# Performance work log

Hardware: AMD Instinct MI355X
Metric: run time of the kernel (lower is better)

Reference implementation:

```python
import jax, jax.numpy as jnp
import numpy as np


def setup_inputs() -> dict:
    key = jax.random.key(0)
    k1, k2, k3, k4 = jax.random.split(key, 4)
    B, T, d_model, d_internal = 4, 2048, 1024, 64
    x = jax.random.normal(k1, (B, T, d_model), dtype=jnp.float32)
    # torch.nn.Linear weights: [out_features, in_features]
    s = 1.0 / np.sqrt(d_model)
    W_Q = jax.random.uniform(k2, (d_internal, d_model), jnp.float32, -s, s)
    W_K = jax.random.uniform(k3, (d_internal, d_model), jnp.float32, -s, s)
    W_V = jax.random.uniform(k4, (d_internal, d_model), jnp.float32, -s, s)
    return {"x": x, "W_Q": W_Q, "W_K": W_K, "W_V": W_V}


def reference(x, W_Q, W_K, W_V):
    B, T, C = x.shape  # C == d_model
    Q = jnp.einsum('btc,dc->btd', x, W_Q)
    K = jnp.einsum('btc,dc->btd', x, W_K)
    # Faithful to source bug: V is computed with W_K, W_V is unused.
    V = jnp.einsum('btc,dc->btd', x, W_K)
    scale = C ** (-0.5)  # source scales by d_model, not d_internal
    attn = jnp.einsum('btd,bsd->bts', Q, K) * scale  # [B,T,T]
    causal = jnp.tril(jnp.ones((T, T), dtype=bool))
    attn = jnp.where(causal[None, :, :], attn, -jnp.inf)
    attn = jax.nn.softmax(attn, axis=-1)
    return jnp.einsum('bts,bsd->btd', attn, V)
```

## Files before the change

kernel.cpp:

```cpp
#include <hip/hip_runtime.h>
#include <hip/hip_bf16.h>
#include <cstdint>
#include <cstddef>

#define BB 4
#define TT 2048
#define DM 1024
#define DH 64

typedef __attribute__((ext_vector_type(8))) short short8;
typedef __attribute__((ext_vector_type(4))) float floatx4;

__device__ __forceinline__ unsigned short f2bf(float f) {
    union { float f; unsigned int u; } v; v.f = f;
    unsigned int u = v.u;
    u += 0x7fffu + ((u >> 16) & 1u);
    return (unsigned short)(u >> 16);
}

__device__ __forceinline__ short8 cvt8(float4 lo, float4 hi) {
    short8 r;
    r[0] = (short)f2bf(lo.x); r[1] = (short)f2bf(lo.y);
    r[2] = (short)f2bf(lo.z); r[3] = (short)f2bf(lo.w);
    r[4] = (short)f2bf(hi.x); r[5] = (short)f2bf(hi.y);
    r[6] = (short)f2bf(hi.z); r[7] = (short)f2bf(hi.w);
    return r;
}

#define WTHREADS (8 * 32 * 64)

__global__ __launch_bounds__(256) void wtile_kernel(const float* __restrict__ wq,
                                                    const float* __restrict__ wk,
                                                    unsigned short* __restrict__ wbt) {
    const int j  = blockIdx.x * 256 + threadIdx.x;
    const int l  = j & 63;
    const int kc = (j >> 6) & 31;
    const int nt = j >> 11;
    const float* wbase = (nt < 4) ? wq : wk;
    const float* src = wbase + (size_t)((nt & 3) * 16 + (l & 15)) * DM
                             + kc * 32 + (l >> 4) * 8;
    float4 a = *reinterpret_cast<const float4*>(src);
    float4 b = *reinterpret_cast<const float4*>(src + 4);
    *reinterpret_cast<short8*>(wbt + (size_t)j * 8) = cvt8(a, b);
}

__global__ __launch_bounds__(256) void proj_kernel(const float* __restrict__ x,
                                                   const unsigned short* __restrict__ wbt,
                                                   unsigned short* __restrict__ qo,
                                                   unsigned short* __restrict__ ko,
                                                   unsigned short* __restrict__ kt) {
    __shared__ __align__(16) unsigned short sA[32 * 64 * 8];

    const int tid  = threadIdx.x;
    const int wave = tid >> 6;
    const int lane = tid & 63;
    const int col  = lane & 15;
    const int quad = lane >> 4;
    const int mt   = blockIdx.x;

    const float* xtile = x + (size_t)mt * 16 * DM;
#pragma unroll 8
    for (int i = 0; i < 8; ++i) {
        const int e  = tid + i * 256;
        const int kc = e >> 6;
        const int l  = e & 63;
        const float* src = xtile + (size_t)(l & 15) * DM + kc * 32 + (l >> 4) * 8;
        float4 a = *reinterpret_cast<const float4*>(src);
        float4 b = *reinterpret_cast<const float4*>(src + 4);
        *reinterpret_cast<short8*>(sA + (size_t)e * 8) = cvt8(a, b);
    }
    __syncthreads();

    const unsigned short* bq = wbt + ((size_t)wave * 32 * 64) * 8;
    const unsigned short* bk = wbt + ((size_t)(4 + wave) * 32 * 64) * 8;

    floatx4 accQ = (floatx4){0.f, 0.f, 0.f, 0.f};
    floatx4 accK = (floatx4){0.f, 0.f, 0.f, 0.f};
#pragma unroll 8
    for (int kc = 0; kc < 32; ++kc) {
        short8 a  = *reinterpret_cast<const short8*>(sA + ((size_t)kc * 64 + lane) * 8);
        short8 b0 = *reinterpret_cast<const short8*>(bq + ((size_t)kc * 64 + lane) * 8);
        short8 b1 = *reinterpret_cast<const short8*>(bk + ((size_t)kc * 64 + lane) * 8);
        accQ = __builtin_amdgcn_mfma_f32_16x16x32_bf16(a, b0, accQ, 0, 0, 0);
        accK = __builtin_amdgcn_mfma_f32_16x16x32_bf16(a, b1, accK, 0, 0, 0);
    }

    const int g = wave * 16 + col;
    unsigned short hk[4];
#pragma unroll
    for (int r = 0; r < 4; ++r) {
        const size_t row = (size_t)(mt * 16 + quad * 4 + r);
        qo[row * DH + g] = f2bf(accQ[r] * 0.03125f);
        hk[r] = f2bf(accK[r]);
        ko[row * DH + g] = hk[r];
    }

    __syncthreads();
    unsigned short* kts = sA;
#pragma unroll
    for (int r = 0; r < 4; ++r)
        kts[g * 16 + quad * 4 + r] = hk[r];
    __syncthreads();
    if (tid < 128) {
        const int d  = tid >> 1;
        const int s8 = (tid & 1) * 8;
        const int b4 = mt >> 7;
        const int s0 = (mt & 127) * 16 + s8;
        short8 v = *reinterpret_cast<const short8*>(kts + d * 16 + s8);
        *reinterpret_cast<short8*>(kt + ((size_t)(b4 * 64 + d)) * TT + s0) = v;
    }
}

__global__ __launch_bounds__(128) void flash1_kernel(const unsigned short* __restrict__ qb,
                                                     const unsigned short* __restrict__ kb,
                                                     const unsigned short* __restrict__ ktb,
                                                     float* __restrict__ Op,
                                                     float* __restrict__ ml) {
    const int c  = blockIdx.x & 15;
    const int qt = (blockIdx.x >> 4) & 63;
    const int b  = blockIdx.x >> 10;
    if (4 * c > qt) return;

    __shared__ __align__(16) unsigned short Pl[2][2][16][40];

    const int tid  = threadIdx.x;
    const int wave = tid >> 6;
    const int lane = tid & 63;
    const int col  = lane & 15;
    const int quad = lane >> 4;

    const int q0    = qt * 32;
    const int qrow  = q0 + wave * 16;
    const int s_beg = c * 128;
    const int s_end = min(s_beg + 128, q0 + 32);

    const unsigned short* qp  = qb  + ((size_t)b * TT + qrow) * DH;
    const unsigned short* kp  = kb  + (size_t)b * TT * DH;
    const unsigned short* ktp = ktb + (size_t)b * 64 * TT;

    short8 qf0 = *reinterpret_cast<const short8*>(qp + (size_t)col * DH + quad * 8);
    short8 qf1 = *reinterpret_cast<const short8*>(qp + (size_t)col * DH + 32 + quad * 8);

    floatx4 o[4];
#pragma unroll
    for (int t = 0; t < 4; ++t) o[t] = (floatx4){0.f, 0.f, 0.f, 0.f};
    float lrow[4] = {0.f, 0.f, 0.f, 0.f};
    int   myq[4];
#pragma unroll
    for (int r = 0; r < 4; ++r) myq[r] = qrow + quad * 4 + r;
    const float LOG2E = 1.44269504f;

    auto body = [&](int s0, int slot) {
        float sv[2][4];
#pragma unroll
        for (int st = 0; st < 2; ++st) {
            const unsigned short* kr = kp + (size_t)(s0 + st * 16 + col) * DH + quad * 8;
            short8 kf0 = *reinterpret_cast<const short8*>(kr);
            short8 kf1 = *reinterpret_cast<const short8*>(kr + 32);
            floatx4 z = (floatx4){0.f, 0.f, 0.f, 0.f};
            z = __builtin_amdgcn_mfma_f32_16x16x32_bf16(qf0, kf0, z, 0, 0, 0);
            z = __builtin_amdgcn_mfma_f32_16x16x32_bf16(qf1, kf1, z, 0, 0, 0);
            const int skey = s0 + st * 16 + col;
#pragma unroll
            for (int r = 0; r < 4; ++r) {
                float p = __builtin_exp2f(z[r] * LOG2E);
                p = (skey <= myq[r]) ? p : 0.f;
                sv[st][r] = p;
                lrow[r] += p;
            }
        }
#pragma unroll
        for (int st = 0; st < 2; ++st)
#pragma unroll
            for (int r = 0; r < 4; ++r)
                Pl[wave][slot][quad * 4 + r][st * 16 + col] = f2bf(sv[st][r]);
        short8 pf = *reinterpret_cast<const short8*>(&Pl[wave][slot][col][quad * 8]);

#pragma unroll
        for (int t = 0; t < 4; ++t) {
            short8 vf = *reinterpret_cast<const short8*>(
                ktp + (size_t)(t * 16 + col) * TT + s0 + quad * 8);
            o[t] = __builtin_amdgcn_mfma_f32_16x16x32_bf16(pf, vf, o[t], 0, 0, 0);
        }
    };

    const int nIter = (s_end - s_beg) >> 5;
    if (nIter == 4) {
        body(s_beg, 0); body(s_beg + 32, 1);
        body(s_beg + 64, 0); body(s_beg + 96, 1);
    } else {
        for (int i = 0; i < nIter; ++i) body(s_beg + 32 * i, i & 1);
    }

#pragma unroll
    for (int m = 1; m < 16; m <<= 1)
#pragma unroll
        for (int r = 0; r < 4; ++r)
            lrow[r] += __shfl_xor(lrow[r], m, 64);

    const int slot = (b * 64 + qt) * 16 + c;
    float* op = Op + (size_t)slot * 2048;
#pragma unroll
    for (int t = 0; t < 4; ++t)
#pragma unroll
        for (int r = 0; r < 4; ++r)
            op[(size_t)(wave * 16 + quad * 4 + r) * DH + t * 16 + col] = o[t][r];
    if (col == 0) {
        float* mlp = ml + (size_t)slot * 32;
#pragma unroll
        for (int r = 0; r < 4; ++r)
            mlp[wave * 16 + quad * 4 + r] = lrow[r];
    }
}

__global__ __launch_bounds__(256) void merge_kernel(const float* __restrict__ Op,
                                                    const float* __restrict__ ml,
                                                    float* __restrict__ out) {
    const int qt  = blockIdx.x & 63;
    const int b   = blockIdx.x >> 6;
    const int nch = (qt >> 2) + 1;
    const int t   = threadIdx.x;
    const int row = t >> 3;
    const int c8  = (t & 7) * 8;
    const size_t base = (size_t)blockIdx.x * 16;

    float L = 0.f;
    float a[8];
#pragma unroll
    for (int i = 0; i < 8; ++i) a[i] = 0.f;
#pragma unroll 4
    for (int c = 0; c < nch; ++c) {
        L += ml[(base + c) * 32 + row];
        const float* op = Op + (base + c) * 2048 + (size_t)row * 64 + c8;
        float4 v0 = *reinterpret_cast<const float4*>(op);
        float4 v1 = *reinterpret_cast<const float4*>(op + 4);
        a[0] += v0.x; a[1] += v0.y; a[2] += v0.z; a[3] += v0.w;
        a[4] += v1.x; a[5] += v1.y; a[6] += v1.z; a[7] += v1.w;
    }
    const float inv = 1.0f / L;
    float* o = out + ((size_t)b * TT + qt * 32 + row) * DH + c8;
    float4 r0 = {a[0] * inv, a[1] * inv, a[2] * inv, a[3] * inv};
    float4 r1 = {a[4] * inv, a[5] * inv, a[6] * inv, a[7] * inv};
    *reinterpret_cast<float4*>(o)     = r0;
    *reinterpret_cast<float4*>(o + 4) = r1;
}

extern "C" void kernel_launch(void* const* d_in, const int* in_sizes, int n_in,
                              void* d_out, int out_size, void* d_ws, size_t ws_size,
                              hipStream_t stream) {
    const float* x  = (const float*)d_in[0];
    const float* wq = (const float*)d_in[1];
    const float* wk = (const float*)d_in[2];

    unsigned short* wbt = (unsigned short*)d_ws;
    unsigned short* qo  = wbt + (size_t)WTHREADS * 8;
    unsigned short* ko  = qo + (size_t)BB * TT * DH;
    unsigned short* kt  = ko + (size_t)BB * TT * DH;
    float* Op = (float*)(kt + (size_t)BB * DH * TT);
    float* ml = Op + (size_t)4096 * 2048;
    float* out = (float*)d_out;

    hipLaunchKernelGGL(wtile_kernel,  dim3(WTHREADS / 256), dim3(256), 0, stream, wq, wk, wbt);
    hipLaunchKernelGGL(proj_kernel,   dim3((BB * TT) / 16), dim3(256), 0, stream, x, wbt, qo, ko, kt);
    hipLaunchKernelGGL(flash1_kernel, dim3(BB * 64 * 16),   dim3(128), 0, stream, qo, ko, kt, Op, ml);
    hipLaunchKernelGGL(merge_kernel,  dim3(BB * 64),        dim3(256), 0, stream, Op, ml, out);
}
```

Measured before the change: 126.7 us.

## Double-buffer x staging in projection and skip causal mask on full tiles

The projection kernel now splits the K dimension into two halves. The second half of x is loaded into registers while MFMAs run on the first half in shared memory, overlapping global loads with compute. The flash kernel applies the causal mask only on the diagonal tile and widens the P staging buffer to four slots, which reduces slot reuse across iterations. This adds register pressure for the prefetched floats and more LDS.

```diff
diff --git a/kernel.cpp b/kernel.cpp
--- a/kernel.cpp
+++ b/kernel.cpp
@@ -49,7 +49,7 @@
                                                    unsigned short* __restrict__ qo,
                                                    unsigned short* __restrict__ ko,
                                                    unsigned short* __restrict__ kt) {
-    __shared__ __align__(16) unsigned short sA[32 * 64 * 8];
+    __shared__ __align__(16) unsigned short sA[2][16 * 64 * 8];
 
     const int tid  = threadIdx.x;
     const int wave = tid >> 6;
@@ -59,28 +59,56 @@
     const int mt   = blockIdx.x;
 
     const float* xtile = x + (size_t)mt * 16 * DM;
-#pragma unroll 8
-    for (int i = 0; i < 8; ++i) {
+    const unsigned short* bq = wbt + ((size_t)wave * 32 * 64) * 8;
+    const unsigned short* bk = wbt + ((size_t)(4 + wave) * 32 * 64) * 8;
+
+    floatx4 accQ = (floatx4){0.f, 0.f, 0.f, 0.f};
+    floatx4 accK = (floatx4){0.f, 0.f, 0.f, 0.f};
+
+#pragma unroll 4
+    for (int i = 0; i < 4; ++i) {
         const int e  = tid + i * 256;
         const int kc = e >> 6;
         const int l  = e & 63;
         const float* src = xtile + (size_t)(l & 15) * DM + kc * 32 + (l >> 4) * 8;
         float4 a = *reinterpret_cast<const float4*>(src);
         float4 b = *reinterpret_cast<const float4*>(src + 4);
-        *reinterpret_cast<short8*>(sA + (size_t)e * 8) = cvt8(a, b);
+        *reinterpret_cast<short8*>(sA[0] + (size_t)e * 8) = cvt8(a, b);
     }
     __syncthreads();
 
-    const unsigned short* bq = wbt + ((size_t)wave * 32 * 64) * 8;
-    const unsigned short* bk = wbt + ((size_t)(4 + wave) * 32 * 64) * 8;
-
-    floatx4 accQ = (floatx4){0.f, 0.f, 0.f, 0.f};
-    floatx4 accK = (floatx4){0.f, 0.f, 0.f, 0.f};
-#pragma unroll 8
-    for (int kc = 0; kc < 32; ++kc) {
-        short8 a  = *reinterpret_cast<const short8*>(sA + ((size_t)kc * 64 + lane) * 8);
+    float4 h1a[4], h1b[4];
+#pragma unroll 4
+    for (int i = 0; i < 4; ++i) {
+        const int e  = tid + i * 256;
+        const int kc = 16 + (e >> 6);
+        const int l  = e & 63;
+        const float* src = xtile + (size_t)(l & 15) * DM + kc * 32 + (l >> 4) * 8;
+        h1a[i] = *reinterpret_cast<const float4*>(src);
+        h1b[i] = *reinterpret_cast<const float4*>(src + 4);
+    }
+
+#pragma unroll
+    for (int kc = 0; kc < 16; ++kc) {
+        short8 a  = *reinterpret_cast<const short8*>(sA[0] + ((size_t)kc * 64 + lane) * 8);
         short8 b0 = *reinterpret_cast<const short8*>(bq + ((size_t)kc * 64 + lane) * 8);
         short8 b1 = *reinterpret_cast<const short8*>(bk + ((size_t)kc * 64 + lane) * 8);
+        accQ = __builtin_amdgcn_mfma_f32_16x16x32_bf16(a, b0, accQ, 0, 0, 0);
+        accK = __builtin_amdgcn_mfma_f32_16x16x32_bf16(a, b1, accK, 0, 0, 0);
+    }
+
+#pragma unroll 4
+    for (int i = 0; i < 4; ++i) {
+        const int e = tid + i * 256;
+        *reinterpret_cast<short8*>(sA[1] + (size_t)e * 8) = cvt8(h1a[i], h1b[i]);
+    }
+    __syncthreads();
+
+#pragma unroll
+    for (int kc = 0; kc < 16; ++kc) {
+        short8 a  = *reinterpret_cast<const short8*>(sA[1] + ((size_t)kc * 64 + lane) * 8);
+        short8 b0 = *reinterpret_cast<const short8*>(bq + ((size_t)(16 + kc) * 64 + lane) * 8);
+        short8 b1 = *reinterpret_cast<const short8*>(bk + ((size_t)(16 + kc) * 64 + lane) * 8);
         accQ = __builtin_amdgcn_mfma_f32_16x16x32_bf16(a, b0, accQ, 0, 0, 0);
         accK = __builtin_amdgcn_mfma_f32_16x16x32_bf16(a, b1, accK, 0, 0, 0);
     }
@@ -96,7 +124,7 @@
     }
 
     __syncthreads();
-    unsigned short* kts = sA;
+    unsigned short* kts = (unsigned short*)sA;
 #pragma unroll
     for (int r = 0; r < 4; ++r)
         kts[g * 16 + quad * 4 + r] = hk[r];
@@ -121,7 +149,7 @@
     const int b  = blockIdx.x >> 10;
     if (4 * c > qt) return;
 
-    __shared__ __align__(16) unsigned short Pl[2][2][16][40];
+    __shared__ __align__(16) unsigned short Pl[2][4][16][40];
 
     const int tid  = threadIdx.x;
     const int wave = tid >> 6;
@@ -150,7 +178,7 @@
     for (int r = 0; r < 4; ++r) myq[r] = qrow + quad * 4 + r;
     const float LOG2E = 1.44269504f;
 
-    auto body = [&](int s0, int slot) {
+    auto body = [&](int s0, int slot, bool domask) {
         float sv[2][4];
 #pragma unroll
         for (int st = 0; st < 2; ++st) {
@@ -164,7 +192,7 @@
 #pragma unroll
             for (int r = 0; r < 4; ++r) {
                 float p = __builtin_exp2f(z[r] * LOG2E);
-                p = (skey <= myq[r]) ? p : 0.f;
+                if (domask) p = (skey <= myq[r]) ? p : 0.f;
                 sv[st][r] = p;
                 lrow[r] += p;
             }
@@ -186,10 +214,15 @@
 
     const int nIter = (s_end - s_beg) >> 5;
     if (nIter == 4) {
-        body(s_beg, 0); body(s_beg + 32, 1);
-        body(s_beg + 64, 0); body(s_beg + 96, 1);
+        body(s_beg,      0, false);
+        body(s_beg + 32, 1, false);
+        body(s_beg + 64, 2, false);
+        body(s_beg + 96, 3, q0 == s_beg + 96);
     } else {
-        for (int i = 0; i < nIter; ++i) body(s_beg + 32 * i, i & 1);
+        for (int i = 0; i < nIter; ++i) {
+            const int s0 = s_beg + 32 * i;
+            body(s0, i & 3, s0 == q0);
+        }
     }
 
 #pragma unroll
```

Result: no change. 127.2 us (+0.4%).
